# Performance work log

Measured on AMD Instinct MI355X. Metric: run time of the kernel, lower is better.

Reference implementation:

```python
import jax, jax.numpy as jnp
import numpy as np
from jax import lax


def conv3x3(x, w):
    # x: (B,C,H,W), w: (O,I,3,3); stride 1, padding 1, no bias
    return lax.conv_general_dilated(x, w, (1, 1), 'SAME',
                                    dimension_numbers=('NCHW', 'OIHW', 'NCHW'))


def group_norm(x, w, b, groups=32, eps=1e-5):
    B, C, H, W = x.shape
    xg = x.reshape(B, groups, C // groups, H, W)
    mu = xg.mean(axis=(2, 3, 4), keepdims=True)
    var = xg.var(axis=(2, 3, 4), keepdims=True)
    xg = (xg - mu) * lax.rsqrt(var + eps)
    return xg.reshape(B, C, H, W) * w[None, :, None, None] + b[None, :, None, None]


def to_patches(x, p1, p2):
    # 'b c (h p1) (w p2) -> (b h w) c (p1 p2)'
    B, C, H, W = x.shape
    h, w = H // p1, W // p2
    x = x.reshape(B, C, h, p1, w, p2).transpose(0, 2, 4, 1, 3, 5)
    return x.reshape(B * h * w, C, p1 * p2)


def from_patches(x, B, h, w, p1, p2):
    # '(b h w) c (p1 p2) -> b c (h p1) (w p2)'
    C = x.shape[1]
    x = x.reshape(B, h, w, C, p1, p2).transpose(0, 3, 1, 4, 2, 5)
    return x.reshape(B, C, h * p1, w * p2)


def setup_inputs() -> dict:
    key = jax.random.key(0)
    ks = jax.random.split(key, 5)
    B, C, H, W = 8, 256, 128, 128
    inter = 256
    s = 0.05  # keep conv outputs in a sane range
    return {
        'x_low': jax.random.normal(ks[0], (B, C, H, W), jnp.float32),
        'x_high': jax.random.normal(ks[1], (B, C, H, W), jnp.float32),
        'w_q': jax.random.normal(ks[2], (inter, C, 3, 3), jnp.float32) * s,
        'gq_w': jnp.ones((inter,), jnp.float32),
        'gq_b': jnp.zeros((inter,), jnp.float32),
        'w_k': jax.random.normal(ks[3], (inter, C, 3, 3), jnp.float32) * s,
        'gk_w': jnp.ones((inter,), jnp.float32),
        'gk_b': jnp.zeros((inter,), jnp.float32),
        'w_o': jax.random.normal(ks[4], (C, inter, 3, 3), jnp.float32) * s,
        'go_w': jnp.ones((C,), jnp.float32),
        'go_b': jnp.zeros((C,), jnp.float32),
        'p1': 8,
        'p2': 8,
    }


def reference(x_low, x_high, w_q, gq_w, gq_b, w_k, gk_w, gk_b, w_o, go_w, go_b, p1, p2):
    B, C, H, W = x_low.shape
    inter = w_q.shape[0]
    h, w = H // p1, W // p2
    # q, k: (B*h*w, inter, T) with T = p1*p2
    q = to_patches(group_norm(conv3x3(x_low, w_q), gq_w, gq_b), p1, p2)
    k = to_patches(group_norm(conv3x3(x_high, w_k), gk_w, gk_b), p1, p2)
    q = q.transpose(0, 2, 1)                                  # (N, T, inter)
    attn = jnp.matmul(q, k) / jnp.sqrt(jnp.float32(inter))    # (N, T, T)
    attn = jax.nn.softmax(attn, axis=-1)
    out = jnp.matmul(attn, k.transpose(0, 2, 1))              # (N, T, inter)
    out = from_patches(out.transpose(0, 2, 1), B, h, w, p1, p2)
    return group_norm(conv3x3(out + x_low, w_o), go_w, go_b)
```

## Files before the change

kernel.cpp:

```cpp
#include <hip/hip_runtime.h>

using u16 = unsigned short;
using u32 = unsigned int;

typedef short bfrag8 __attribute__((ext_vector_type(8)));
typedef float f32x4  __attribute__((ext_vector_type(4)));

__device__ __forceinline__ void unpack8(const int4 v, float f[8]) {
  u32 a = (u32)v.x, b = (u32)v.y, c = (u32)v.z, d = (u32)v.w;
  f[0] = __uint_as_float(a << 16);
  f[1] = __uint_as_float(a & 0xffff0000u);
  f[2] = __uint_as_float(b << 16);
  f[3] = __uint_as_float(b & 0xffff0000u);
  f[4] = __uint_as_float(c << 16);
  f[5] = __uint_as_float(c & 0xffff0000u);
  f[6] = __uint_as_float(d << 16);
  f[7] = __uint_as_float(d & 0xffff0000u);
}

__device__ __forceinline__ u16 f2bf(float f) {
  u32 u = __float_as_uint(f);
  u32 r = u + 0x7fffu + ((u >> 16) & 1u);
  return (u16)(r >> 16);
}

__device__ __forceinline__ void gload_lds16(const void* g, void* l) {
  __builtin_amdgcn_global_load_lds(
      (const __attribute__((address_space(1))) void*)g,
      (__attribute__((address_space(3))) void*)l, 16, 0, 0);
}

__global__ __launch_bounds__(256) void wprep(
    const float* __restrict__ wq, const float* __restrict__ wk, const float* __restrict__ wo,
    u16* __restrict__ dq, u16* __restrict__ dk, u16* __restrict__ dwo)
{
  const float* s = (blockIdx.y == 0) ? wq : (blockIdx.y == 1) ? wk : wo;
  u16* d = (blockIdx.y == 0) ? dq : (blockIdx.y == 1) ? dk : dwo;
  int id = blockIdx.x * 256 + threadIdx.x;
  int e = id * 4;
  int tap = e >> 16;
  int rem = e & 65535;
  int oc = rem >> 8, ic = rem & 255;
  u16 o[4];
#pragma unroll
  for (int j = 0; j < 4; ++j)
    o[j] = f2bf(s[((size_t)oc * 256 + ic + j) * 9 + tap]);
  *reinterpret_cast<uint2*>(d + e) = *reinterpret_cast<uint2*>(o);
}

__global__ __launch_bounds__(256) void xpose(
    const float* __restrict__ xa, const float* __restrict__ xb,
    u16* __restrict__ oa, u16* __restrict__ ob)
{
  const int row = blockIdx.x, b = blockIdx.y;
  const float* src = blockIdx.z ? xb : xa;
  u16* dst = blockIdx.z ? ob : oa;
  const int t = threadIdx.x;
  const int px4 = (t >> 3) * 4;
  const int c8 = (t & 7) * 8;
#pragma unroll
  for (int p = 0; p < 4; ++p) {
    int c0 = p * 64 + c8;
    float4 v[8];
#pragma unroll
    for (int j = 0; j < 8; ++j)
      v[j] = *reinterpret_cast<const float4*>(src + ((size_t)b * 256 + c0 + j) * 16384 + row * 128 + px4);
#pragma unroll
    for (int e = 0; e < 4; ++e) {
      u16 o[8];
      o[0] = f2bf(e==0?v[0].x:e==1?v[0].y:e==2?v[0].z:v[0].w);
      o[1] = f2bf(e==0?v[1].x:e==1?v[1].y:e==2?v[1].z:v[1].w);
      o[2] = f2bf(e==0?v[2].x:e==1?v[2].y:e==2?v[2].z:v[2].w);
      o[3] = f2bf(e==0?v[3].x:e==1?v[3].y:e==2?v[3].z:v[3].w);
      o[4] = f2bf(e==0?v[4].x:e==1?v[4].y:e==2?v[4].z:v[4].w);
      o[5] = f2bf(e==0?v[5].x:e==1?v[5].y:e==2?v[5].z:v[5].w);
      o[6] = f2bf(e==0?v[6].x:e==1?v[6].y:e==2?v[6].z:v[6].w);
      o[7] = f2bf(e==0?v[7].x:e==1?v[7].y:e==2?v[7].z:v[7].w);
      *reinterpret_cast<int4*>(dst + (((size_t)b * 128 + row) * 128 + px4 + e) * 256 + c0) =
          *reinterpret_cast<int4*>(o);
    }
  }
}

__global__ __launch_bounds__(256, 3) void conv_mfma(
    const u16* __restrict__ X, const u16* __restrict__ W2, u16* __restrict__ Y)
{
  __shared__ __attribute__((aligned(16))) char csm[41728];

  const int t = threadIdx.x;
  const int lane = t & 63;
  const int wv = t >> 6;
  const int oc0 = blockIdx.x * 128;
  const int y0 = blockIdx.y;
  const int bb = blockIdx.z;
  const int och = wv >> 1, pxh = wv & 1;
  const int lc = lane & 15, lq = lane >> 4;

  f32x4 acc[4][4];
#pragma unroll
  for (int m = 0; m < 4; ++m)
#pragma unroll
    for (int n = 0; n < 4; ++n) acc[m][n] = (f32x4){0.f, 0.f, 0.f, 0.f};

  const size_t xplane = (size_t)bb * (128 * 128 * 256);

  {
    int4 z = {0, 0, 0, 0};
    if (t < 24) {
      int q = t & 3, sel = (t >> 2) & 1, kh = t >> 3;
      int cidx = sel ? 129 : 0;
      *reinterpret_cast<int4*>(csm + ((kh * 132 + cidx) * 4 + q) * 16) = z;
    }
    if (y0 == 0)
      for (int s = t; s < 528; s += 256) *reinterpret_cast<int4*>(csm + s * 16) = z;
    if (y0 == 127)
      for (int s = t; s < 528; s += 256) *reinterpret_cast<int4*>(csm + 16896 + s * 16) = z;
  }

  auto stageA = [&](int tap, int buf, int ic0) {
#pragma unroll
    for (int i = 0; i < 2; ++i) {
      int idx = t + i * 256;
      const u16* src = W2 + (((size_t)(tap * 256 + oc0 + (idx >> 2))) << 8) + ic0 + (idx & 3) * 8;
      gload_lds16(src, csm + 25344 + buf * 8192 + (i * 256 + (t & ~63)) * 16);
    }
  };
  auto stageB = [&](int ic0) {
#pragma unroll
    for (int i = 0; i < 6; ++i) {
      int idx = t + i * 256;
      int kh = idx >> 9;
      int row = y0 - 1 + kh;
      if (row >= 0 && row < 128) {
        int px = (idx & 511) >> 2, q = idx & 3;
        const u16* src = X + xplane + (((size_t)(row * 128 + px)) << 8) + ic0 + q * 8;
        gload_lds16(src, csm + 64 + kh * 256 + (i * 256 + (t & ~63)) * 16);
      }
    }
  };

  stageB(0);
  stageA(0, 0, 0);
  __syncthreads();

  for (int chunk = 0; chunk < 8; ++chunk) {
    const int ic0 = chunk * 32;
#pragma unroll
    for (int tap = 0; tap < 9; ++tap) {
      const int kh = tap / 3, kw = tap % 3, buf = tap & 1;
      if (tap < 8) stageA(tap + 1, buf ^ 1, ic0);
      bfrag8 af[4], xf[4];
#pragma unroll
      for (int m = 0; m < 4; ++m)
        af[m] = *reinterpret_cast<const bfrag8*>(csm + 25344 + buf * 8192 +
                    ((och * 64 + m * 16 + lc) * 4 + lq) * 16);
#pragma unroll
      for (int n = 0; n < 4; ++n)
        xf[n] = *reinterpret_cast<const bfrag8*>(csm + kh * 8448 + kw * 64 +
                    ((pxh * 64 + n * 16 + lc) * 64 + lq * 16));
#pragma unroll
      for (int m = 0; m < 4; ++m)
#pragma unroll
        for (int n = 0; n < 4; ++n)
          acc[m][n] = __builtin_amdgcn_mfma_f32_16x16x32_bf16(af[m], xf[n], acc[m][n], 0, 0, 0);
      __syncthreads();
    }
    if (chunk < 7) {
      stageB(ic0 + 32);
      stageA(0, 0, ic0 + 32);
      __syncthreads();
    }
  }

  u16* Ost = (u16*)csm;
  const int chb = och * 64 + lq * 4;
  const int pxb = pxh * 64 + lc;
#pragma unroll
  for (int m = 0; m < 4; ++m)
#pragma unroll
    for (int n = 0; n < 4; ++n) {
      u32 lo = (u32)f2bf(acc[m][n][0]) | ((u32)f2bf(acc[m][n][1]) << 16);
      u32 hi = (u32)f2bf(acc[m][n][2]) | ((u32)f2bf(acc[m][n][3]) << 16);
      uint2 pk = {lo, hi};
      *reinterpret_cast<uint2*>(&Ost[(pxb + n * 16) * 136 + chb + m * 16]) = pk;
    }
  __syncthreads();
#pragma unroll
  for (int s = 0; s < 8; ++s) {
    int pix = s * 16 + (t >> 4);
    int sub = t & 15;
    int4 v = *reinterpret_cast<const int4*>(&Ost[pix * 136 + sub * 8]);
    *reinterpret_cast<int4*>(Y + xplane + (((size_t)(y0 * 128 + pix)) << 8) + oc0 + sub * 8) = v;
  }
}

__global__ __launch_bounds__(256) void gnstat1(const u16* __restrict__ Y, float* __restrict__ part)
{
  const int chunk = blockIdx.x, b = blockIdx.y;
  const int t = threadIdx.x;
  const int c8 = (t & 31) * 8;
  const int pr = t >> 5;
  float s[8], ss[8];
#pragma unroll
  for (int j = 0; j < 8; ++j) { s[j] = 0.f; ss[j] = 0.f; }
  for (int i = 0; i < 64; ++i) {
    int p = chunk * 512 + pr + i * 8;
    int4 v = *reinterpret_cast<const int4*>(Y + ((size_t)b * 16384 + p) * 256 + c8);
    float f[8]; unpack8(v, f);
#pragma unroll
    for (int j = 0; j < 8; ++j) { s[j] += f[j]; ss[j] = fmaf(f[j], f[j], ss[j]); }
  }
  __shared__ float L[8][256];
#pragma unroll
  for (int j = 0; j < 8; ++j) L[pr][c8 + j] = s[j];
  __syncthreads();
  float sv = 0.f;
#pragma unroll
  for (int r = 0; r < 8; ++r) sv += L[r][t];
  __syncthreads();
#pragma unroll
  for (int j = 0; j < 8; ++j) L[pr][c8 + j] = ss[j];
  __syncthreads();
  float ssv = 0.f;
#pragma unroll
  for (int r = 0; r < 8; ++r) ssv += L[r][t];
  part[(((size_t)b * 32 + chunk) * 256 + t) * 2 + 0] = sv;
  part[(((size_t)b * 32 + chunk) * 256 + t) * 2 + 1] = ssv;
}

__global__ __launch_bounds__(256) void gnstat2(const float* __restrict__ part, float* __restrict__ stat)
{
  const int b = blockIdx.x, t = threadIdx.x;
  float s = 0.f, ss = 0.f;
  for (int ch = 0; ch < 32; ++ch) {
    s  += part[(((size_t)b * 32 + ch) * 256 + t) * 2 + 0];
    ss += part[(((size_t)b * 32 + ch) * 256 + t) * 2 + 1];
  }
  __shared__ float Ls[256], Lss[256];
  Ls[t] = s; Lss[t] = ss;
  __syncthreads();
  if (t < 32) {
    float S = 0.f, SS = 0.f;
#pragma unroll
    for (int j = 0; j < 8; ++j) { S += Ls[t * 8 + j]; SS += Lss[t * 8 + j]; }
    float mean = S * (1.f / 131072.f);
    float var = SS * (1.f / 131072.f) - mean * mean;
    stat[b * 32 + t] = mean;
    stat[256 + b * 32 + t] = rsqrtf(var + 1e-5f);
  }
}

__global__ __launch_bounds__(256) void normq(
    u16* __restrict__ yq, const float* __restrict__ statq, const float* __restrict__ statk,
    const float* __restrict__ gqw, const float* __restrict__ gqb, const float* __restrict__ gkw)
{
  const int row = blockIdx.x, b = blockIdx.y;
  const int t = threadIdx.x;
#pragma unroll
  for (int i = 0; i < 16; ++i) {
    int idx = i * 256 + t;
    int c8 = (idx & 31) * 8;
    int g = c8 >> 3;
    float meanq = statq[b * 32 + g], rstdq = statq[256 + b * 32 + g];
    float rstdk = statk[256 + b * 32 + g];
    size_t off = (((size_t)b * 128 + row) * 128 + (idx >> 5)) * 256 + c8;
    int4 v = *reinterpret_cast<const int4*>(yq + off);
    float f[8]; unpack8(v, f);
    u16 o[8];
#pragma unroll
    for (int j = 0; j < 8; ++j) {
      float Aq = rstdq * gqw[c8 + j];
      float Bq = gqb[c8 + j] - meanq * Aq;
      float Ak = rstdk * gkw[c8 + j];
      o[j] = f2bf((f[j] * Aq + Bq) * Ak);
    }
    *reinterpret_cast<int4*>(yq + off) = *reinterpret_cast<int4*>(o);
  }
}

__global__ __launch_bounds__(256) void normkT(
    const u16* __restrict__ yk, const float* __restrict__ statk,
    const float* __restrict__ gkw, const float* __restrict__ gkb,
    u16* __restrict__ kT)
{
  __shared__ u16 L[8][264];
  const int y = blockIdx.x, b = blockIdx.y;
  const int ph = y >> 3, py = y & 7;
  const int t = threadIdx.x;
  const int px = t >> 5, c8 = (t & 31) * 8;
  const int g = c8 >> 3;
  float mean = statk[b * 32 + g], rstd = statk[256 + b * 32 + g];
  float A[8], Bv[8];
#pragma unroll
  for (int j = 0; j < 8; ++j) {
    A[j] = rstd * gkw[c8 + j];
    Bv[j] = gkb[c8 + j] - mean * A[j];
  }
  const size_t rowbase = (((size_t)b * 128 + y) * 128) * 256;
  const size_t outbase = ((size_t)(b * 16 + ph) * 8 + py) * 32768;
  for (int pw = 0; pw < 16; ++pw) {
    int4 v = *reinterpret_cast<const int4*>(yk + rowbase + (size_t)(pw * 8 + px) * 256 + c8);
    float f[8]; unpack8(v, f);
    u16 o[8];
#pragma unroll
    for (int j = 0; j < 8; ++j) o[j] = f2bf(f[j] * A[j] + Bv[j]);
    *reinterpret_cast<int4*>(&L[px][c8]) = *reinterpret_cast<int4*>(o);
    __syncthreads();
    u16 o2[8];
#pragma unroll
    for (int q = 0; q < 8; ++q) o2[q] = L[q][t];
    *reinterpret_cast<int4*>(kT + outbase + (size_t)(pw * 256 + t) * 8) = *reinterpret_cast<int4*>(o2);
    __syncthreads();
  }
}

#define OST 280
__global__ __launch_bounds__(256, 3) void attn_mfma(
    const u16* __restrict__ qt, const u16* __restrict__ yk,
    const u16* __restrict__ kT, const u16* __restrict__ xl,
    u16* __restrict__ resid)
{
  __shared__ __attribute__((aligned(16))) u16 smem[64 * OST + 4 * 16 * 72];
  u16* Ost = smem;
  u16* Pls = smem + 64 * OST;

  const int n = blockIdx.x;
  const int b = n >> 8, ph = (n >> 4) & 15, pw = n & 15;
  const int t = threadIdx.x, l = t & 63, w = t >> 6;
  const int lc = l & 15, lg = l >> 4;

  auto tokaddr = [&](int tok) -> size_t {
    return (((size_t)(b * 128 + ph * 8 + (tok >> 3))) * 128 + pw * 8 + (tok & 7)) * 256;
  };

  const size_t qa = tokaddr(16 * w + lc) + lg * 8;
  bfrag8 aF[8];
#pragma unroll
  for (int ks = 0; ks < 8; ++ks)
    aF[ks] = *reinterpret_cast<const bfrag8*>(qt + qa + ks * 32);

  f32x4 sacc[4];
#pragma unroll
  for (int nt = 0; nt < 4; ++nt) sacc[nt] = (f32x4){0.f, 0.f, 0.f, 0.f};

#pragma unroll
  for (int nt = 0; nt < 4; ++nt) {
    const size_t ka = tokaddr(nt * 16 + lc) + lg * 8;
    bfrag8 bF[8];
#pragma unroll
    for (int ks = 0; ks < 8; ++ks)
      bF[ks] = *reinterpret_cast<const bfrag8*>(yk + ka + ks * 32);
#pragma unroll
    for (int ks = 0; ks < 8; ++ks)
      sacc[nt] = __builtin_amdgcn_mfma_f32_16x16x32_bf16(aF[ks], bF[ks], sacc[nt], 0, 0, 0);
  }

  u16* Pw = Pls + w * (16 * 72);
#pragma unroll
  for (int r = 0; r < 4; ++r) {
    float m0 = fmaxf(fmaxf(sacc[0][r], sacc[1][r]), fmaxf(sacc[2][r], sacc[3][r]));
    m0 = fmaxf(m0, __shfl_xor(m0, 1));
    m0 = fmaxf(m0, __shfl_xor(m0, 2));
    m0 = fmaxf(m0, __shfl_xor(m0, 4));
    m0 = fmaxf(m0, __shfl_xor(m0, 8));
    float p0 = __expf((sacc[0][r] - m0) * 0.0625f);
    float p1 = __expf((sacc[1][r] - m0) * 0.0625f);
    float p2 = __expf((sacc[2][r] - m0) * 0.0625f);
    float p3 = __expf((sacc[3][r] - m0) * 0.0625f);
    float s0 = p0 + p1 + p2 + p3;
    s0 += __shfl_xor(s0, 1);
    s0 += __shfl_xor(s0, 2);
    s0 += __shfl_xor(s0, 4);
    s0 += __shfl_xor(s0, 8);
    float inv = 1.f / s0;
    int prow = (lg * 4 + r) * 72;
    Pw[prow + 0 * 16 + lc] = f2bf(p0 * inv);
    Pw[prow + 1 * 16 + lc] = f2bf(p1 * inv);
    Pw[prow + 2 * 16 + lc] = f2bf(p2 * inv);
    Pw[prow + 3 * 16 + lc] = f2bf(p3 * inv);
  }

  bfrag8 pA[2];
#pragma unroll
  for (int js = 0; js < 2; ++js)
    pA[js] = *reinterpret_cast<const bfrag8*>(Pw + lc * 72 + js * 32 + lg * 8);

  f32x4 pacc[16];
#pragma unroll
  for (int ct = 0; ct < 16; ++ct) pacc[ct] = (f32x4){0.f, 0.f, 0.f, 0.f};

#pragma unroll
  for (int ct = 0; ct < 16; ++ct) {
    bfrag8 vB[2];
#pragma unroll
    for (int js = 0; js < 2; ++js)
      vB[js] = *reinterpret_cast<const bfrag8*>(
          kT + ((size_t)((b * 16 + ph) * 8 + js * 4 + lg)) * 32768 +
          (size_t)(pw * 256 + ct * 16 + lc) * 8);
#pragma unroll
    for (int js = 0; js < 2; ++js)
      pacc[ct] = __builtin_amdgcn_mfma_f32_16x16x32_bf16(pA[js], vB[js], pacc[ct], 0, 0, 0);
  }

#pragma unroll
  for (int ct = 0; ct < 16; ++ct)
#pragma unroll
    for (int r = 0; r < 4; ++r)
      Ost[(16 * w + lg * 4 + r) * OST + ct * 16 + lc] = f2bf(pacc[ct][r]);
  __syncthreads();

#pragma unroll
  for (int s = 0; s < 8; ++s) {
    int px_ = t >> 5;
    int c16 = t & 31;
    size_t g = (((size_t)b * 128 + ph * 8 + s) * 128 + pw * 8 + px_) * 256 + c16 * 8;
    int4 o = *reinterpret_cast<const int4*>(&Ost[(s * 8 + px_) * OST + c16 * 8]);
    int4 r = *reinterpret_cast<const int4*>(xl + g);
    float fo[8], fr[8]; unpack8(o, fo); unpack8(r, fr);
    u16 pk[8];
#pragma unroll
    for (int j = 0; j < 8; ++j) pk[j] = f2bf(fo[j] + fr[j]);
    *reinterpret_cast<int4*>(resid + g) = *reinterpret_cast<int4*>(pk);
  }
}

__global__ __launch_bounds__(256) void gnapply_t(
    const u16* __restrict__ Y, const float* __restrict__ stat,
    const float* __restrict__ gw, const float* __restrict__ gb,
    float* __restrict__ out)
{
  const int row = blockIdx.x, b = blockIdx.y;
  const int t = threadIdx.x;
  const int px4 = (t & 31) * 4;
  const int c8 = (t >> 5) * 8;
#pragma unroll
  for (int p = 0; p < 4; ++p) {
    int c0 = p * 64 + c8;
    int g = c0 >> 3;
    float mean = stat[b * 32 + g], rstd = stat[256 + b * 32 + g];
    float A[8], Bv[8];
#pragma unroll
    for (int j = 0; j < 8; ++j) {
      A[j] = rstd * gw[c0 + j];
      Bv[j] = gb[c0 + j] - mean * A[j];
    }
    float vals[4][8];
#pragma unroll
    for (int e = 0; e < 4; ++e) {
      int4 v = *reinterpret_cast<const int4*>(Y + (((size_t)b * 128 + row) * 128 + px4 + e) * 256 + c0);
      float f[8]; unpack8(v, f);
#pragma unroll
      for (int j = 0; j < 8; ++j) vals[e][j] = fmaf(f[j], A[j], Bv[j]);
    }
#pragma unroll
    for (int j = 0; j < 8; ++j) {
      float4 o = {vals[0][j], vals[1][j], vals[2][j], vals[3][j]};
      *reinterpret_cast<float4*>(out + ((size_t)b * 256 + c0 + j) * 16384 + row * 128 + px4) = o;
    }
  }
}

extern "C" void kernel_launch(void* const* d_in, const int* in_sizes, int n_in,
                              void* d_out, int out_size, void* d_ws, size_t ws_size,
                              hipStream_t stream)
{
  const float* x_low  = (const float*)d_in[0];
  const float* x_high = (const float*)d_in[1];
  const float* w_q    = (const float*)d_in[2];
  const float* gq_w   = (const float*)d_in[3];
  const float* gq_b   = (const float*)d_in[4];
  const float* w_k    = (const float*)d_in[5];
  const float* gk_w   = (const float*)d_in[6];
  const float* gk_b   = (const float*)d_in[7];
  const float* w_o    = (const float*)d_in[8];
  const float* go_w   = (const float*)d_in[9];
  const float* go_b   = (const float*)d_in[10];
  float* out = (float*)d_out;

  char* ws = (char*)d_ws;
  const size_t slot = 67108864;
  u16* xl  = (u16*)(ws + 0 * slot);
  u16* xh  = (u16*)(ws + 1 * slot);
  u16* yq  = (u16*)(ws + 2 * slot);
  u16* yk  = (u16*)(ws + 3 * slot);
  u16* kT  = (u16*)(ws + 4 * slot);
  u16* W2q = (u16*)(ws + 5 * slot);
  u16* W2k = W2q + 589824;
  u16* W2o = W2k + 589824;
  float* partq = (float*)(ws + 5 * slot + 3 * 1179648);
  float* partk = partq + 131072;
  float* statq = partk + 131072;
  float* statk = statq + 512;
  float* stato = statk + 512;

  wprep<<<dim3(576, 3), 256, 0, stream>>>(w_q, w_k, w_o, W2q, W2k, W2o);
  xpose<<<dim3(128, 8, 2), 256, 0, stream>>>(x_low, x_high, xl, xh);
  conv_mfma<<<dim3(2, 128, 8), 256, 0, stream>>>(xl, W2q, yq);
  conv_mfma<<<dim3(2, 128, 8), 256, 0, stream>>>(xh, W2k, yk);
  gnstat1<<<dim3(32, 8), 256, 0, stream>>>(yq, partq);
  gnstat1<<<dim3(32, 8), 256, 0, stream>>>(yk, partk);
  gnstat2<<<8, 256, 0, stream>>>(partq, statq);
  gnstat2<<<8, 256, 0, stream>>>(partk, statk);
  normq<<<dim3(128, 8), 256, 0, stream>>>(yq, statq, statk, gq_w, gq_b, gk_w);
  normkT<<<dim3(128, 8), 256, 0, stream>>>(yk, statk, gk_w, gk_b, kT);
  attn_mfma<<<2048, 256, 0, stream>>>(yq, yk, kT, xl, xh);
  conv_mfma<<<dim3(2, 128, 8), 256, 0, stream>>>(xh, W2o, xl);
  gnstat1<<<dim3(32, 8), 256, 0, stream>>>(xl, partq);
  gnstat2<<<8, 256, 0, stream>>>(partq, stato);
  gnapply_t<<<dim3(128, 8), 256, 0, stream>>>(xl, stato, go_w, go_b, out);
}
```

Baseline: 798.1 us.

## Fuse GroupNorm stats into conv epilogue and q-normalization into attention

The conv kernel now uses 512-thread blocks that cover all 256 output channels of one row, so each input row is staged once instead of twice. Its epilogue computes per-channel partial sums and sums of squares from the fp32 accumulators with lane shuffles, which removes the separate gnstat1 passes over the conv outputs. The q GroupNorm plus k-scale normalization moves into the attention kernel's q-fragment load, dropping the normq read-modify-write pass. In exchange the conv block needs much more LDS and more waves per block, which may reduce occupancy. Statistics now come from unrounded fp32 values rather than bf16-rounded outputs.

```diff
diff --git a/kernel.cpp b/kernel.cpp
--- a/kernel.cpp
+++ b/kernel.cpp
@@ -82,19 +82,20 @@
   }
 }
 
-__global__ __launch_bounds__(256, 3) void conv_mfma(
-    const u16* __restrict__ X, const u16* __restrict__ W2, u16* __restrict__ Y)
-{
-  __shared__ __attribute__((aligned(16))) char csm[41728];
+__global__ __launch_bounds__(512, 4) void conv_mfma(
+    const u16* __restrict__ X, const u16* __restrict__ W2, u16* __restrict__ Y,
+    float* __restrict__ part)
+{
+  __shared__ __attribute__((aligned(16))) char csm[71680];
 
   const int t = threadIdx.x;
-  const int lane = t & 63;
+  const int l = t & 63;
   const int wv = t >> 6;
-  const int oc0 = blockIdx.x * 128;
-  const int y0 = blockIdx.y;
-  const int bb = blockIdx.z;
+  const int id = blockIdx.x;
+  const int u = (id & 7) * 128 + (id >> 3);
+  const int bb = u >> 7, y0 = u & 127;
   const int och = wv >> 1, pxh = wv & 1;
-  const int lc = lane & 15, lq = lane >> 4;
+  const int lc = l & 15, lq = l >> 4;
 
   f32x4 acc[4][4];
 #pragma unroll
@@ -112,29 +113,29 @@
       *reinterpret_cast<int4*>(csm + ((kh * 132 + cidx) * 4 + q) * 16) = z;
     }
     if (y0 == 0)
-      for (int s = t; s < 528; s += 256) *reinterpret_cast<int4*>(csm + s * 16) = z;
+      for (int s = t; s < 528; s += 512) *reinterpret_cast<int4*>(csm + s * 16) = z;
     if (y0 == 127)
-      for (int s = t; s < 528; s += 256) *reinterpret_cast<int4*>(csm + 16896 + s * 16) = z;
+      for (int s = t; s < 528; s += 512) *reinterpret_cast<int4*>(csm + 16896 + s * 16) = z;
   }
 
   auto stageA = [&](int tap, int buf, int ic0) {
 #pragma unroll
     for (int i = 0; i < 2; ++i) {
-      int idx = t + i * 256;
-      const u16* src = W2 + (((size_t)(tap * 256 + oc0 + (idx >> 2))) << 8) + ic0 + (idx & 3) * 8;
-      gload_lds16(src, csm + 25344 + buf * 8192 + (i * 256 + (t & ~63)) * 16);
+      int idx = t + i * 512;
+      const u16* src = W2 + (((size_t)(tap * 256 + (idx >> 2))) << 8) + ic0 + (idx & 3) * 8;
+      gload_lds16(src, csm + 25344 + buf * 16384 + (i * 512 + (t & ~63)) * 16);
     }
   };
   auto stageB = [&](int ic0) {
 #pragma unroll
-    for (int i = 0; i < 6; ++i) {
-      int idx = t + i * 256;
+    for (int i = 0; i < 3; ++i) {
+      int idx = t + i * 512;
       int kh = idx >> 9;
       int row = y0 - 1 + kh;
       if (row >= 0 && row < 128) {
         int px = (idx & 511) >> 2, q = idx & 3;
         const u16* src = X + xplane + (((size_t)(row * 128 + px)) << 8) + ic0 + q * 8;
-        gload_lds16(src, csm + 64 + kh * 256 + (i * 256 + (t & ~63)) * 16);
+        gload_lds16(src, csm + 64 + kh * 256 + (i * 512 + (t & ~63)) * 16);
       }
     }
   };
@@ -152,7 +153,7 @@
       bfrag8 af[4], xf[4];
 #pragma unroll
       for (int m = 0; m < 4; ++m)
-        af[m] = *reinterpret_cast<const bfrag8*>(csm + 25344 + buf * 8192 +
+        af[m] = *reinterpret_cast<const bfrag8*>(csm + 25344 + buf * 16384 +
                     ((och * 64 + m * 16 + lc) * 4 + lq) * 16);
 #pragma unroll
       for (int n = 0; n < 4; ++n)
@@ -173,6 +174,7 @@
   }
 
   u16* Ost = (u16*)csm;
+  float* sst = (float*)(csm + 67584);
   const int chb = och * 64 + lq * 4;
   const int pxb = pxh * 64 + lc;
 #pragma unroll
@@ -182,59 +184,52 @@
       u32 lo = (u32)f2bf(acc[m][n][0]) | ((u32)f2bf(acc[m][n][1]) << 16);
       u32 hi = (u32)f2bf(acc[m][n][2]) | ((u32)f2bf(acc[m][n][3]) << 16);
       uint2 pk = {lo, hi};
-      *reinterpret_cast<uint2*>(&Ost[(pxb + n * 16) * 136 + chb + m * 16]) = pk;
+      *reinterpret_cast<uint2*>(&Ost[(pxb + n * 16) * 264 + chb + m * 16]) = pk;
+    }
+#pragma unroll
+  for (int m = 0; m < 4; ++m)
+#pragma unroll
+    for (int r = 0; r < 4; ++r) {
+      float s  = acc[m][0][r] + acc[m][1][r] + acc[m][2][r] + acc[m][3][r];
+      float ss = acc[m][0][r] * acc[m][0][r] + acc[m][1][r] * acc[m][1][r] +
+                 acc[m][2][r] * acc[m][2][r] + acc[m][3][r] * acc[m][3][r];
+#pragma unroll
+      for (int off = 1; off < 16; off <<= 1) {
+        s  += __shfl_xor(s, off);
+        ss += __shfl_xor(ss, off);
+      }
+      if (lc == 0) {
+        int c = och * 64 + m * 16 + lq * 4 + r;
+        sst[pxh * 512 + c]       = s;
+        sst[pxh * 512 + 256 + c] = ss;
+      }
     }
   __syncthreads();
-#pragma unroll
-  for (int s = 0; s < 8; ++s) {
-    int pix = s * 16 + (t >> 4);
-    int sub = t & 15;
-    int4 v = *reinterpret_cast<const int4*>(&Ost[pix * 136 + sub * 8]);
-    *reinterpret_cast<int4*>(Y + xplane + (((size_t)(y0 * 128 + pix)) << 8) + oc0 + sub * 8) = v;
-  }
-}
-
-__global__ __launch_bounds__(256) void gnstat1(const u16* __restrict__ Y, float* __restrict__ part)
-{
-  const int chunk = blockIdx.x, b = blockIdx.y;
-  const int t = threadIdx.x;
-  const int c8 = (t & 31) * 8;
-  const int pr = t >> 5;
-  float s[8], ss[8];
-#pragma unroll
-  for (int j = 0; j < 8; ++j) { s[j] = 0.f; ss[j] = 0.f; }
-  for (int i = 0; i < 64; ++i) {
-    int p = chunk * 512 + pr + i * 8;
-    int4 v = *reinterpret_cast<const int4*>(Y + ((size_t)b * 16384 + p) * 256 + c8);
-    float f[8]; unpack8(v, f);
-#pragma unroll
-    for (int j = 0; j < 8; ++j) { s[j] += f[j]; ss[j] = fmaf(f[j], f[j], ss[j]); }
-  }
-  __shared__ float L[8][256];
-#pragma unroll
-  for (int j = 0; j < 8; ++j) L[pr][c8 + j] = s[j];
-  __syncthreads();
-  float sv = 0.f;
-#pragma unroll
-  for (int r = 0; r < 8; ++r) sv += L[r][t];
-  __syncthreads();
-#pragma unroll
-  for (int j = 0; j < 8; ++j) L[pr][c8 + j] = ss[j];
-  __syncthreads();
-  float ssv = 0.f;
-#pragma unroll
-  for (int r = 0; r < 8; ++r) ssv += L[r][t];
-  part[(((size_t)b * 32 + chunk) * 256 + t) * 2 + 0] = sv;
-  part[(((size_t)b * 32 + chunk) * 256 + t) * 2 + 1] = ssv;
-}
-
-__global__ __launch_bounds__(256) void gnstat2(const float* __restrict__ part, float* __restrict__ stat)
+
+  if (t < 256) {
+    float s  = sst[t]       + sst[512 + t];
+    float ss = sst[256 + t] + sst[768 + t];
+    size_t pb = (((size_t)bb * 128 + y0) * 256 + t) * 2;
+    part[pb]     = s;
+    part[pb + 1] = ss;
+  }
+#pragma unroll
+  for (int s8 = 0; s8 < 8; ++s8) {
+    int pix = s8 * 16 + (t >> 5);
+    int sub = t & 31;
+    int4 v = *reinterpret_cast<const int4*>(&Ost[pix * 264 + sub * 8]);
+    *reinterpret_cast<int4*>(Y + xplane + (((size_t)(y0 * 128 + pix)) << 8) + sub * 8) = v;
+  }
+}
+
+__global__ __launch_bounds__(256) void gnstat2b(const float* __restrict__ part, float* __restrict__ stat)
 {
   const int b = blockIdx.x, t = threadIdx.x;
   float s = 0.f, ss = 0.f;
-  for (int ch = 0; ch < 32; ++ch) {
-    s  += part[(((size_t)b * 32 + ch) * 256 + t) * 2 + 0];
-    ss += part[(((size_t)b * 32 + ch) * 256 + t) * 2 + 1];
+  for (int row = 0; row < 128; ++row) {
+    size_t pb = (((size_t)b * 128 + row) * 256 + t) * 2;
+    s  += part[pb];
+    ss += part[pb + 1];
   }
   __shared__ float Ls[256], Lss[256];
   Ls[t] = s; Lss[t] = ss;
@@ -247,34 +242,6 @@
     float var = SS * (1.f / 131072.f) - mean * mean;
     stat[b * 32 + t] = mean;
     stat[256 + b * 32 + t] = rsqrtf(var + 1e-5f);
-  }
-}
-
-__global__ __launch_bounds__(256) void normq(
-    u16* __restrict__ yq, const float* __restrict__ statq, const float* __restrict__ statk,
-    const float* __restrict__ gqw, const float* __restrict__ gqb, const float* __restrict__ gkw)
-{
-  const int row = blockIdx.x, b = blockIdx.y;
-  const int t = threadIdx.x;
-#pragma unroll
-  for (int i = 0; i < 16; ++i) {
-    int idx = i * 256 + t;
-    int c8 = (idx & 31) * 8;
-    int g = c8 >> 3;
-    float meanq = statq[b * 32 + g], rstdq = statq[256 + b * 32 + g];
-    float rstdk = statk[256 + b * 32 + g];
-    size_t off = (((size_t)b * 128 + row) * 128 + (idx >> 5)) * 256 + c8;
-    int4 v = *reinterpret_cast<const int4*>(yq + off);
-    float f[8]; unpack8(v, f);
-    u16 o[8];
-#pragma unroll
-    for (int j = 0; j < 8; ++j) {
-      float Aq = rstdq * gqw[c8 + j];
-      float Bq = gqb[c8 + j] - meanq * Aq;
-      float Ak = rstdk * gkw[c8 + j];
-      o[j] = f2bf((f[j] * Aq + Bq) * Ak);
-    }
-    *reinterpret_cast<int4*>(yq + off) = *reinterpret_cast<int4*>(o);
   }
 }
 
@@ -316,8 +283,11 @@
 
 #define OST 280
 __global__ __launch_bounds__(256, 3) void attn_mfma(
-    const u16* __restrict__ qt, const u16* __restrict__ yk,
+    const u16* __restrict__ yq, const u16* __restrict__ yk,
     const u16* __restrict__ kT, const u16* __restrict__ xl,
+    const float* __restrict__ statq, const float* __restrict__ statk,
+    const float* __restrict__ gqw, const float* __restrict__ gqb,
+    const float* __restrict__ gkw,
     u16* __restrict__ resid)
 {
   __shared__ __attribute__((aligned(16))) u16 smem[64 * OST + 4 * 16 * 72];
@@ -336,8 +306,32 @@
   const size_t qa = tokaddr(16 * w + lc) + lg * 8;
   bfrag8 aF[8];
 #pragma unroll
-  for (int ks = 0; ks < 8; ++ks)
-    aF[ks] = *reinterpret_cast<const bfrag8*>(qt + qa + ks * 32);
+  for (int ks = 0; ks < 8; ++ks) {
+    int c0 = lg * 8 + ks * 32;
+    int g = ks * 4 + lg;
+    float meanq = statq[b * 32 + g], rstdq = statq[256 + b * 32 + g];
+    float rstdk = statk[256 + b * 32 + g];
+    int4 v = *reinterpret_cast<const int4*>(yq + qa + ks * 32);
+    float f[8]; unpack8(v, f);
+    float4 w0 = *reinterpret_cast<const float4*>(gqw + c0);
+    float4 w1 = *reinterpret_cast<const float4*>(gqw + c0 + 4);
+    float4 b0 = *reinterpret_cast<const float4*>(gqb + c0);
+    float4 b1 = *reinterpret_cast<const float4*>(gqb + c0 + 4);
+    float4 k0 = *reinterpret_cast<const float4*>(gkw + c0);
+    float4 k1 = *reinterpret_cast<const float4*>(gkw + c0 + 4);
+    float ww[8] = {w0.x, w0.y, w0.z, w0.w, w1.x, w1.y, w1.z, w1.w};
+    float bb[8] = {b0.x, b0.y, b0.z, b0.w, b1.x, b1.y, b1.z, b1.w};
+    float kk[8] = {k0.x, k0.y, k0.z, k0.w, k1.x, k1.y, k1.z, k1.w};
+    u16 o[8];
+#pragma unroll
+    for (int j = 0; j < 8; ++j) {
+      float Aq = rstdq * ww[j];
+      float Bq = bb[j] - meanq * Aq;
+      float Ak = rstdk * kk[j];
+      o[j] = f2bf((f[j] * Aq + Bq) * Ak);
+    }
+    aF[ks] = *reinterpret_cast<bfrag8*>(o);
+  }
 
   f32x4 sacc[4];
 #pragma unroll
@@ -488,24 +482,22 @@
   u16* W2k = W2q + 589824;
   u16* W2o = W2k + 589824;
   float* partq = (float*)(ws + 5 * slot + 3 * 1179648);
-  float* partk = partq + 131072;
-  float* statq = partk + 131072;
+  float* partk = partq + 524288;
+  float* parto = partk + 524288;
+  float* statq = parto + 524288;
   float* statk = statq + 512;
   float* stato = statk + 512;
 
   wprep<<<dim3(576, 3), 256, 0, stream>>>(w_q, w_k, w_o, W2q, W2k, W2o);
   xpose<<<dim3(128, 8, 2), 256, 0, stream>>>(x_low, x_high, xl, xh);
-  conv_mfma<<<dim3(2, 128, 8), 256, 0, stream>>>(xl, W2q, yq);
-  conv_mfma<<<dim3(2, 128, 8), 256, 0, stream>>>(xh, W2k, yk);
-  gnstat1<<<dim3(32, 8), 256, 0, stream>>>(yq, partq);
-  gnstat1<<<dim3(32, 8), 256, 0, stream>>>(yk, partk);
-  gnstat2<<<8, 256, 0, stream>>>(partq, statq);
-  gnstat2<<<8, 256, 0, stream>>>(partk, statk);
-  normq<<<dim3(128, 8), 256, 0, stream>>>(yq, statq, statk, gq_w, gq_b, gk_w);
+  conv_mfma<<<1024, 512, 0, stream>>>(xl, W2q, yq, partq);
+  conv_mfma<<<1024, 512, 0, stream>>>(xh, W2k, yk, partk);
+  gnstat2b<<<8, 256, 0, stream>>>(partq, statq);
+  gnstat2b<<<8, 256, 0, stream>>>(partk, statk);
   normkT<<<dim3(128, 8), 256, 0, stream>>>(yk, statk, gk_w, gk_b, kT);
-  attn_mfma<<<2048, 256, 0, stream>>>(yq, yk, kT, xl, xh);
-  conv_mfma<<<dim3(2, 128, 8), 256, 0, stream>>>(xh, W2o, xl);
-  gnstat1<<<dim3(32, 8), 256, 0, stream>>>(xl, partq);
-  gnstat2<<<8, 256, 0, stream>>>(partq, stato);
+  attn_mfma<<<2048, 256, 0, stream>>>(yq, yk, kT, xl, statq, statk,
+                                      gq_w, gq_b, gk_w, xh);
+  conv_mfma<<<1024, 512, 0, stream>>>(xh, W2o, xl, parto);
+  gnstat2b<<<8, 256, 0, stream>>>(parto, stato);
   gnapply_t<<<dim3(128, 8), 256, 0, stream>>>(xl, stato, go_w, go_b, out);
 }
```

New measurement: 693.7 us. -13.1%, faster.
